# Kernel tuning notes

Measured on AMD Instinct MI355X. Metric: run time of the kernel, lower is better.

Reference implementation:

```python
import jax, jax.numpy as jnp
import numpy as np

B, C, H, W = 32, 1536, 24, 24
HID, D, K = 512, 128, 64  # hidden, cluster_dim, num_clusters


def setup_inputs() -> dict:
    key = jax.random.key(0)
    ks = jax.random.split(key, 6)
    def rn(k, shape, scale):
        return jax.random.normal(k, shape, dtype=jnp.float32) * scale
    return {
        "x": rn(ks[0], (B, C, H, W), 1.0),
        # cluster_features: Conv2d(C,512,1) -> ReLU -> Conv2d(512,D,1)
        "w1c": rn(ks[1], (HID, C), 0.02), "b1c": jnp.zeros((HID,), jnp.float32),
        "w2c": rn(ks[2], (D, HID), 0.02), "b2c": jnp.zeros((D,), jnp.float32),
        # score: Conv2d(C,512,1) -> ReLU -> Conv2d(512,K,1)
        "w1s": rn(ks[3], (HID, C), 0.02), "b1s": jnp.zeros((HID,), jnp.float32),
        "w2s": rn(ks[4], (K, HID), 0.02), "b2s": jnp.zeros((K,), jnp.float32),
        "temperature": jnp.array(1.0, jnp.float32),
    }


def _sinkhorn_log(S, num_iters=3):
    # log-domain OT solver with uniform marginals log(1/n), reg=1 (M/reg == M)
    b, m, n = S.shape
    norm = -jnp.log(jnp.asarray(n, S.dtype))
    log_a = jnp.full((b, m), norm, S.dtype)
    log_b = jnp.full((b, n), norm, S.dtype)
    u = jnp.zeros((b, m), S.dtype)
    v = jnp.zeros((b, n), S.dtype)
    for _ in range(num_iters):
        u = log_a - jax.nn.logsumexp(S + v[:, None, :], axis=2)
        v = log_b - jax.nn.logsumexp(S + u[:, :, None], axis=1)
    # get_matching_probs subtracts norm at the end
    return S + u[:, :, None] + v[:, None, :] - norm


def reference(x, w1c, b1c, w2c, b2c, w1s, b1s, w2s, b2s, temperature):
    b, c, h, w = x.shape
    xf = x.reshape(b, c, h * w)  # (B, C, N); 1x1 conv == channel GEMM
    # cluster features f: (B, D, N)
    hc = jax.nn.relu(jnp.einsum('oc,bcn->bon', w1c, xf) + b1c[None, :, None])
    f = jnp.einsum('oc,bcn->bon', w2c, hc) + b2c[None, :, None]
    # assignment scores p: (B, K, N)
    hs = jax.nn.relu(jnp.einsum('oc,bcn->bon', w1s, xf) + b1s[None, :, None])
    s = jnp.einsum('oc,bcn->bon', w2s, hs) + b2s[None, :, None]
    log_p = _sinkhorn_log(s, num_iters=3)
    p = jnp.exp(log_p / temperature) + jnp.exp(log_p)  # (B, K, N)
    # (f.unsqueeze(2) * p.unsqueeze(1)).sum(-1) == batched matmul
    agg = jnp.einsum('bcn,bkn->bck', f, p)  # (B, D, K)
    flat = agg.reshape(b, -1)
    nrm = jnp.maximum(jnp.linalg.norm(flat, axis=-1, keepdims=True), 1e-12)
    return flat / nrm
```

## Files before the change

kernel.cpp:

```cpp
#include <hip/hip_runtime.h>

typedef unsigned short ushort_t;
typedef float f32x4 __attribute__((ext_vector_type(4)));
typedef short short8 __attribute__((ext_vector_type(8)));

#define B_   32
#define C_   1536
#define N_   576
#define HID_ 512
#define D_   128
#define K_   64

__device__ __forceinline__ float bf2f(ushort_t u) {
    union { unsigned u; float f; } c; c.u = ((unsigned)u) << 16; return c.f;
}
__device__ __forceinline__ ushort_t f2bf(float x) {
    unsigned u = __float_as_uint(x);
    return (ushort_t)((u + 0x7FFFu + ((u >> 16) & 1u)) >> 16);
}

typedef const __attribute__((address_space(1))) char gas_char;
typedef __attribute__((address_space(3))) char las_char;
__device__ __forceinline__ void cp16(const void* g, void* l) {
    __builtin_amdgcn_global_load_lds((gas_char*)(size_t)g,
                                     (las_char*)(unsigned)(size_t)l, 16, 0, 0);
}
__device__ __forceinline__ void bar() {
    asm volatile("" ::: "memory");
    __builtin_amdgcn_s_barrier();
    asm volatile("" ::: "memory");
}

#define OB1_  1572864
#define OW2C_ 1573888
#define OB2C_ 1639424
#define OW2S_ 1639552
#define OB2S_ 1672320
#define WTOT_ 1672384
#define TRB2_ 3456
#define CVB4_ (((WTOT_ / 4) + 255) / 256)

__global__ __launch_bounds__(256) void prep_kernel(
    const void* __restrict__ x,
    const void* __restrict__ w1c, const void* __restrict__ b1c,
    const void* __restrict__ w2c, const void* __restrict__ b2c,
    const void* __restrict__ w1s, const void* __restrict__ b1s,
    const void* __restrict__ w2s, const void* __restrict__ b2s,
    const unsigned* __restrict__ temp,
    ushort_t* __restrict__ xt, ushort_t* __restrict__ o, float* __restrict__ Tp)
{
    __shared__ ushort_t t[128][65];
    unsigned d = temp[0];
    int flag = (d == 0x3F800000u) ? 1 : 0;
    int tid = threadIdx.x;
    int idx = blockIdx.x;
    if (idx == 0 && tid == 0)
        *Tp = flag ? __uint_as_float(d) : bf2f((ushort_t)(d & 0xFFFFu));

    if (idx < TRB2_) {
        int b = idx / 108, rem = idx % 108;
        int c0 = (rem % 12) * 128, n0 = (rem / 12) * 64;
        ushort_t* xtb = xt + (size_t)b * N_ * C_;
        int r = tid >> 4, n4 = (tid & 15) * 4;
        if (flag) {
            const float* xb = (const float*)x + (size_t)b * C_ * N_;
#pragma unroll
            for (int i = 0; i < 8; ++i) {
                int cc = r + i * 16;
                float4 v = *(const float4*)&xb[(size_t)(c0 + cc) * N_ + n0 + n4];
                t[cc][n4 + 0] = f2bf(v.x);
                t[cc][n4 + 1] = f2bf(v.y);
                t[cc][n4 + 2] = f2bf(v.z);
                t[cc][n4 + 3] = f2bf(v.w);
            }
        } else {
            const ushort_t* xb = (const ushort_t*)x + (size_t)b * C_ * N_;
#pragma unroll
            for (int i = 0; i < 8; ++i) {
                int cc = r + i * 16;
                *(uint2*)&t[cc][n4] =
                    *(const uint2*)&xb[(size_t)(c0 + cc) * N_ + n0 + n4];
            }
        }
        __syncthreads();
        int c8 = (tid & 15) * 8;
#pragma unroll
        for (int i = 0; i < 4; ++i) {
            int nn = r + i * 16;
            ushort_t vv[8];
#pragma unroll
            for (int j = 0; j < 8; ++j) vv[j] = t[c8 + j][nn];
            uint4 o4;
            o4.x = (unsigned)vv[0] | ((unsigned)vv[1] << 16);
            o4.y = (unsigned)vv[2] | ((unsigned)vv[3] << 16);
            o4.z = (unsigned)vv[4] | ((unsigned)vv[5] << 16);
            o4.w = (unsigned)vv[6] | ((unsigned)vv[7] << 16);
            *(uint4*)&xtb[(size_t)(n0 + nn) * C_ + c0 + c8] = o4;
        }
    } else {
        int i4 = ((idx - TRB2_) * 256 + tid) * 4;
        if (i4 >= WTOT_) return;
        const void* p; int off;
        if      (i4 < 786432)  { p = w1c; off = i4; }
        else if (i4 < OB1_)    { p = w1s; off = i4 - 786432; }
        else if (i4 < 1573376) { p = b1c; off = i4 - OB1_; }
        else if (i4 < OW2C_)   { p = b1s; off = i4 - 1573376; }
        else if (i4 < OB2C_)   { p = w2c; off = i4 - OW2C_; }
        else if (i4 < OW2S_)   { p = b2c; off = i4 - OB2C_; }
        else if (i4 < OB2S_)   { p = w2s; off = i4 - OW2S_; }
        else                   { p = b2s; off = i4 - OB2S_; }
        if (flag) {
            float4 v = *(const float4*)((const float*)p + off);
            uint2 r;
            r.x = (unsigned)f2bf(v.x) | ((unsigned)f2bf(v.y) << 16);
            r.y = (unsigned)f2bf(v.z) | ((unsigned)f2bf(v.w) << 16);
            *(uint2*)&o[i4] = r;
        } else {
            *(uint2*)&o[i4] = *(const uint2*)((const ushort_t*)p + off);
        }
    }
}

__global__ __launch_bounds__(256) void gemm1_kernel(
    const ushort_t* __restrict__ Xt, const ushort_t* __restrict__ W1,
    const ushort_t* __restrict__ bias, ushort_t* __restrict__ h)
{
    __shared__ ushort_t Atile[2][128 * 64];
    __shared__ ushort_t Btile[2][128 * 64];
    int idx = blockIdx.x;
    int l = (idx & 7) * 144 + (idx >> 3);
    int mt = l >> 3, t = l & 7;
    int row0 = mt * 128, col0 = t * 128;

    int tid = threadIdx.x, w = tid >> 6, lane = tid & 63;
    int wr = w >> 1, wc = w & 1;
    int r16 = lane & 15, q = lane >> 4, kh = q * 8;

    int srow = tid >> 3;
    int cx = ((tid & 7) ^ (srow & 7)) * 8;
    const ushort_t* ag[4];
    const ushort_t* bg[4];
#pragma unroll
    for (int s = 0; s < 4; ++s) {
        ag[s] = Xt + (size_t)(row0 + s * 32 + srow) * C_ + cx;
        bg[s] = W1 + (size_t)(col0 + s * 32 + srow) * C_ + cx;
    }

    f32x4 acc[4][4];
#pragma unroll
    for (int i = 0; i < 4; ++i)
#pragma unroll
        for (int j = 0; j < 4; ++j) acc[i][j] = f32x4{0.f, 0.f, 0.f, 0.f};

    int rowa = wr * 64 + r16;
    int rowb = wc * 64 + r16;
    int xr = (r16 & 7) * 8;

    auto stage = [&](int buf, int koff) {
#pragma unroll
        for (int s = 0; s < 4; ++s) {
            cp16(ag[s] + koff, &Atile[buf][tid * 8 + s * 2048]);
            cp16(bg[s] + koff, &Btile[buf][tid * 8 + s * 2048]);
        }
    };
    auto compute = [&](int cb) {
#pragma unroll
        for (int ks = 0; ks < 2; ++ks) {
            int ke = (ks * 32 + kh) ^ xr;
            short8 af[4], bf[4];
#pragma unroll
            for (int i = 0; i < 4; ++i)
                af[i] = *(const short8*)&Atile[cb][(rowa + i * 16) * 64 + ke];
#pragma unroll
            for (int j = 0; j < 4; ++j)
                bf[j] = *(const short8*)&Btile[cb][(rowb + j * 16) * 64 + ke];
#pragma unroll
            for (int i = 0; i < 4; ++i)
#pragma unroll
                for (int j = 0; j < 4; ++j)
                    acc[i][j] = __builtin_amdgcn_mfma_f32_16x16x32_bf16(
                        af[i], bf[j], acc[i][j], 0, 0, 0);
        }
    };

    stage(0, 0);
#pragma unroll
    for (int kt = 0; kt < 24; ++kt) {
        int buf = kt & 1;
        if (kt < 23) {
            stage(buf ^ 1, (kt + 1) * 64);
            asm volatile("s_waitcnt vmcnt(8)" ::: "memory");
        } else {
            asm volatile("s_waitcnt vmcnt(0)" ::: "memory");
        }
        bar();
        compute(buf);
        bar();
    }

#pragma unroll
    for (int j = 0; j < 4; ++j) {
        int col = col0 + wc * 64 + j * 16 + r16;
        float cb = bf2f(bias[col]);
#pragma unroll
        for (int i = 0; i < 4; ++i) {
            int rowo = row0 + wr * 64 + i * 16 + q * 4;
#pragma unroll
            for (int r = 0; r < 4; ++r) {
                float v = fmaxf(acc[i][j][r] + cb, 0.f);
                h[(size_t)(rowo + r) * 1024 + col] = f2bf(v);
            }
        }
    }
}

__global__ __launch_bounds__(256) void gemm2_kernel(
    const ushort_t* __restrict__ Wb, const ushort_t* __restrict__ h,
    ushort_t* __restrict__ fbuf, float* __restrict__ sbuf)
{
    __shared__ ushort_t Atile[2][128 * 32];
    __shared__ ushort_t Btile[2][128 * 32];
    int nt = blockIdx.x, b = blockIdx.y, z = blockIdx.z;
    int col0 = nt * 128;
    int Mclamp = z ? K_ : D_;
    const ushort_t* Aw   = Wb + (z ? OW2S_ : OW2C_);
    const ushort_t* bias = Wb + (z ? OB2S_ : OB2C_);
    const ushort_t* hb = h + (size_t)b * N_ * 1024 + (z ? 512 : 0);

    int tid = threadIdx.x, w = tid >> 6, lane = tid & 63;
    int wr = w >> 1, wc = w & 1;
    int r16 = lane & 15, q = lane >> 4, kh = q * 8;

    int srow = tid >> 2;
    int swz = ((tid & 3) ^ (srow & 3)) * 8;
    int ar0 = min(srow, Mclamp - 1);
    int ar1 = min(64 + srow, Mclamp - 1);
    const ushort_t* ag0 = Aw + (size_t)ar0 * HID_ + swz;
    const ushort_t* ag1 = Aw + (size_t)ar1 * HID_ + swz;
    int br0 = min(col0 + srow, N_ - 1);
    int br1 = min(col0 + 64 + srow, N_ - 1);
    const ushort_t* bg0 = hb + (size_t)br0 * 1024 + swz;
    const ushort_t* bg1 = hb + (size_t)br1 * 1024 + swz;

    f32x4 acc[4][4];
#pragma unroll
    for (int i = 0; i < 4; ++i)
#pragma unroll
        for (int j = 0; j < 4; ++j) acc[i][j] = f32x4{0.f, 0.f, 0.f, 0.f};

    int xr = (r16 & 3) * 8;

    auto stage = [&](int buf, int koff) {
        cp16(ag0 + koff, &Atile[buf][tid * 8]);
        cp16(ag1 + koff, &Atile[buf][2048 + tid * 8]);
        cp16(bg0 + koff, &Btile[buf][tid * 8]);
        cp16(bg1 + koff, &Btile[buf][2048 + tid * 8]);
    };
    auto compute = [&](int cb) {
        int ke = kh ^ xr;
        short8 af[4], bf[4];
#pragma unroll
        for (int i = 0; i < 4; ++i)
            af[i] = *(const short8*)&Atile[cb][(wr * 64 + i * 16 + r16) * 32 + ke];
#pragma unroll
        for (int j = 0; j < 4; ++j)
            bf[j] = *(const short8*)&Btile[cb][(wc * 64 + j * 16 + r16) * 32 + ke];
#pragma unroll
        for (int i = 0; i < 4; ++i)
#pragma unroll
            for (int j = 0; j < 4; ++j)
                acc[i][j] = __builtin_amdgcn_mfma_f32_16x16x32_bf16(
                    af[i], bf[j], acc[i][j], 0, 0, 0);
    };

    stage(0, 0);
#pragma unroll
    for (int kt = 0; kt < 16; ++kt) {
        int buf = kt & 1;
        if (kt < 15) {
            stage(buf ^ 1, (kt + 1) * 32);
            asm volatile("s_waitcnt vmcnt(4)" ::: "memory");
        } else {
            asm volatile("s_waitcnt vmcnt(0)" ::: "memory");
        }
        bar();
        compute(buf);
        bar();
    }

#pragma unroll
    for (int j = 0; j < 4; ++j) {
        int col = col0 + wc * 64 + j * 16 + r16;
#pragma unroll
        for (int i = 0; i < 4; ++i) {
            int rowb = wr * 64 + i * 16 + q * 4;
#pragma unroll
            for (int r = 0; r < 4; ++r) {
                int rr = rowb + r;
                if (rr < Mclamp && col < N_) {
                    float v = acc[i][j][r] + bf2f(bias[rr]);
                    if (z == 0)
                        fbuf[(size_t)b * D_ * N_ + (size_t)rr * N_ + col] = f2bf(v);
                    else
                        sbuf[(size_t)b * K_ * N_ + (size_t)rr * N_ + col] = v;
                }
            }
        }
    }
}

__global__ __launch_bounds__(512) void sinkhorn_kernel(
    const float* __restrict__ s_all, const float* __restrict__ Tp,
    ushort_t* __restrict__ P_all)
{
    int b = blockIdx.x;
    const float* S = s_all + (size_t)b * K_ * N_;
    __shared__ float Sl[K_ * 577];
    __shared__ float su[K_];
    __shared__ float sv[N_];
    int tid = threadIdx.x, w = tid >> 6, lane = tid & 63;
    const float norm = -logf((float)N_);

    const float4* S4 = (const float4*)S;
    for (int g = tid; g < (K_ * N_) / 4; g += 512) {
        float4 v = S4[g];
        int w0 = g * 4;
        int r = w0 / N_;
        int base = w0 + r;
        Sl[base + 0] = v.x; Sl[base + 1] = v.y;
        Sl[base + 2] = v.z; Sl[base + 3] = v.w;
    }
    for (int n = tid; n < N_; n += 512) sv[n] = 0.f;
    __syncthreads();

    for (int it = 0; it < 3; ++it) {
        for (int r = w; r < K_; r += 8) {
            const float* Sr = Sl + r * 577;
            float a0 = 0.f, a1 = 0.f, a2 = 0.f;
#pragma unroll
            for (int k = 0; k < 9; k += 3) {
                int n0 = lane + 64 * k;
                a0 += __expf(Sr[n0] + sv[n0]);
                a1 += __expf(Sr[n0 + 64] + sv[n0 + 64]);
                a2 += __expf(Sr[n0 + 128] + sv[n0 + 128]);
            }
            float t = a0 + a1 + a2;
#pragma unroll
            for (int off = 32; off; off >>= 1) t += __shfl_xor(t, off);
            if (lane == 0) su[r] = norm - __logf(t);
        }
        __syncthreads();
        for (int n = tid; n < N_; n += 512) {
            const float* Sc = Sl + n;
            float a0 = 0.f, a1 = 0.f, a2 = 0.f, a3 = 0.f;
#pragma unroll
            for (int m = 0; m < K_; m += 4) {
                a0 += __expf(Sc[(m + 0) * 577] + su[m + 0]);
                a1 += __expf(Sc[(m + 1) * 577] + su[m + 1]);
                a2 += __expf(Sc[(m + 2) * 577] + su[m + 2]);
                a3 += __expf(Sc[(m + 3) * 577] + su[m + 3]);
            }
            sv[n] = norm - __logf((a0 + a1) + (a2 + a3));
        }
        __syncthreads();
    }

    float invT = 1.f / (*Tp);
    ushort_t* Pb = P_all + (size_t)b * K_ * N_;
    for (int r = w; r < K_; r += 8) {
        float ur = su[r];
        const float* Sr = Sl + r * 577;
#pragma unroll
        for (int k = 0; k < 9; ++k) {
            int n0 = lane + 64 * k;
            float lp = Sr[n0] + ur + sv[n0] - norm;
            Pb[r * N_ + n0] = f2bf(__expf(lp * invT) + __expf(lp));
        }
    }
}

__global__ __launch_bounds__(256) void aggnorm_kernel(
    const ushort_t* __restrict__ f_all, const ushort_t* __restrict__ P_all,
    const unsigned* __restrict__ temp, void* __restrict__ out)
{
    __shared__ ushort_t Atile[2][128 * 64];
    __shared__ ushort_t Ptile[2][64 * 64];
    __shared__ float red[4];
    int b = blockIdx.x;
    const ushort_t* F = f_all + (size_t)b * D_ * N_;
    const ushort_t* P = P_all + (size_t)b * K_ * N_;
    int tid = threadIdx.x, w = tid >> 6, lane = tid & 63;
    int wr = w >> 1, wc = w & 1;
    int r16 = lane & 15, q = lane >> 4, kh = q * 8;

    int srow = tid >> 3;
    int cx = ((tid & 7) ^ (srow & 7)) * 8;
    const ushort_t* fg[4];
    const ushort_t* pg[2];
#pragma unroll
    for (int s = 0; s < 4; ++s)
        fg[s] = F + (size_t)(s * 32 + srow) * N_ + cx;
#pragma unroll
    for (int s = 0; s < 2; ++s)
        pg[s] = P + (size_t)(s * 32 + srow) * N_ + cx;

    f32x4 acc[4][2];
#pragma unroll
    for (int i = 0; i < 4; ++i)
#pragma unroll
        for (int j = 0; j < 2; ++j) acc[i][j] = f32x4{0.f, 0.f, 0.f, 0.f};

    int rowa = wr * 64 + r16;
    int rowp = wc * 32 + r16;
    int xr = (r16 & 7) * 8;

    auto stage = [&](int buf, int koff) {
#pragma unroll
        for (int s = 0; s < 4; ++s)
            cp16(fg[s] + koff, &Atile[buf][tid * 8 + s * 2048]);
#pragma unroll
        for (int s = 0; s < 2; ++s)
            cp16(pg[s] + koff, &Ptile[buf][tid * 8 + s * 2048]);
    };
    auto compute = [&](int cb) {
#pragma unroll
        for (int ks = 0; ks < 2; ++ks) {
            int ke = (ks * 32 + kh) ^ xr;
            short8 af[4], pf[2];
#pragma unroll
            for (int i = 0; i < 4; ++i)
                af[i] = *(const short8*)&Atile[cb][(rowa + i * 16) * 64 + ke];
#pragma unroll
            for (int j = 0; j < 2; ++j)
                pf[j] = *(const short8*)&Ptile[cb][(rowp + j * 16) * 64 + ke];
#pragma unroll
            for (int i = 0; i < 4; ++i)
#pragma unroll
                for (int j = 0; j < 2; ++j)
                    acc[i][j] = __builtin_amdgcn_mfma_f32_16x16x32_bf16(
                        af[i], pf[j], acc[i][j], 0, 0, 0);
        }
    };

    stage(0, 0);
#pragma unroll
    for (int kt = 0; kt < 9; ++kt) {
        int buf = kt & 1;
        if (kt < 8) {
            stage(buf ^ 1, (kt + 1) * 64);
            asm volatile("s_waitcnt vmcnt(6)" ::: "memory");
        } else {
            asm volatile("s_waitcnt vmcnt(0)" ::: "memory");
        }
        bar();
        compute(buf);
        bar();
    }

    float ssq = 0.f;
#pragma unroll
    for (int i = 0; i < 4; ++i)
#pragma unroll
        for (int j = 0; j < 2; ++j)
#pragma unroll
            for (int r = 0; r < 4; ++r) { float v = acc[i][j][r]; ssq += v * v; }
#pragma unroll
    for (int off = 32; off; off >>= 1) ssq += __shfl_xor(ssq, off);
    if (lane == 0) red[w] = ssq;
    __syncthreads();
    float tot = red[0] + red[1] + red[2] + red[3];
    float inv = 1.f / fmaxf(sqrtf(tot), 1e-12f);
    int flag = (temp[0] == 0x3F800000u) ? 1 : 0;
#pragma unroll
    for (int i = 0; i < 4; ++i) {
#pragma unroll
        for (int j = 0; j < 2; ++j) {
            int col = wc * 32 + j * 16 + r16;
#pragma unroll
            for (int r = 0; r < 4; ++r) {
                int row = wr * 64 + i * 16 + q * 4 + r;
                float v = acc[i][j][r] * inv;
                size_t idx = (size_t)b * D_ * K_ + (size_t)row * K_ + col;
                if (flag) ((float*)out)[idx] = v;
                else      ((ushort_t*)out)[idx] = f2bf(v);
            }
        }
    }
}

extern "C" void kernel_launch(void* const* d_in, const int* in_sizes, int n_in,
                              void* d_out, int out_size, void* d_ws, size_t ws_size,
                              hipStream_t stream) {
    const void* x    = d_in[0];
    const void* w1c  = d_in[1];
    const void* b1c  = d_in[2];
    const void* w2c  = d_in[3];
    const void* b2c  = d_in[4];
    const void* w1s  = d_in[5];
    const void* b1s  = d_in[6];
    const void* w2s  = d_in[7];
    const void* b2s  = d_in[8];
    const unsigned* temp = (const unsigned*)d_in[9];

    char* ws = (char*)d_ws;
    float* Tp = (float*)ws;
    ushort_t* Wb = (ushort_t*)(ws + 256);
    size_t offXt = 256 + (((size_t)WTOT_ * 2 + 255) & ~(size_t)255);
    ushort_t* Xt = (ushort_t*)(ws + offXt);
    size_t xtBytes = (size_t)B_ * N_ * C_ * 2;
    ushort_t* h  = (ushort_t*)(ws + offXt + xtBytes);
    size_t o0 = offXt;
    ushort_t* fbuf = (ushort_t*)(ws + o0);  o0 += (size_t)B_ * D_ * N_ * 2;
    float*    sbuf = (float*)(ws + o0);     o0 += (size_t)B_ * K_ * N_ * 4;
    ushort_t* Pws  = (ushort_t*)(ws + o0);  o0 += (size_t)B_ * K_ * N_ * 2;

    prep_kernel<<<dim3(TRB2_ + CVB4_), 256, 0, stream>>>(
        x, w1c, b1c, w2c, b2c, w1s, b1s, w2s, b2s, temp, Xt, Wb, Tp);
    gemm1_kernel<<<dim3(1152), 256, 0, stream>>>(Xt, Wb, Wb + OB1_, h);
    gemm2_kernel<<<dim3(5, B_, 2), 256, 0, stream>>>(Wb, h, fbuf, sbuf);
    sinkhorn_kernel<<<dim3(B_), 512, 0, stream>>>(sbuf, Tp, Pws);
    aggnorm_kernel<<<dim3(B_), 256, 0, stream>>>(fbuf, Pws, temp, (void*)d_out);
}
```

Before: 302.4 us.

## Fuse Sinkhorn and aggregation-normalize kernels into one tail kernel

Merges the Sinkhorn kernel and the aggregation/normalization GEMM into a single 512-thread kernel per batch. The P matrix is kept in registers, then written into LDS by reusing the S buffer, instead of going through global memory. Only F tiles are streamed with double-buffered async copies. This removes one launch and the global round trip for P, at the cost of a larger LDS footprint. The GEMM is still limited to one block per batch, 32 blocks in total.

After: 302.9 us. Within noise of the previous version (+0.2%).

```diff
diff --git a/kernel.cpp b/kernel.cpp
--- a/kernel.cpp
+++ b/kernel.cpp
@@ -309,19 +309,24 @@
     }
 }
 
-__global__ __launch_bounds__(512) void sinkhorn_kernel(
-    const float* __restrict__ s_all, const float* __restrict__ Tp,
-    ushort_t* __restrict__ P_all)
+__global__ __launch_bounds__(512) void tail_kernel(
+    const ushort_t* __restrict__ f_all, const float* __restrict__ s_all,
+    const float* __restrict__ Tp, const unsigned* __restrict__ temp,
+    void* __restrict__ out)
 {
-    int b = blockIdx.x;
-    const float* S = s_all + (size_t)b * K_ * N_;
     __shared__ float Sl[K_ * 577];
     __shared__ float su[K_];
     __shared__ float sv[N_];
+    __shared__ float red[8];
+    ushort_t* Plds = (ushort_t*)Sl;
+    ushort_t* At0  = (ushort_t*)((char*)Sl + 81920);
+    ushort_t* At1  = (ushort_t*)((char*)Sl + 81920 + 16384);
+
+    int b = blockIdx.x;
     int tid = threadIdx.x, w = tid >> 6, lane = tid & 63;
     const float norm = -logf((float)N_);
 
-    const float4* S4 = (const float4*)S;
+    const float4* S4 = (const float4*)(s_all + (size_t)b * K_ * N_);
     for (int g = tid; g < (K_ * N_) / 4; g += 512) {
         float4 v = S4[g];
         int w0 = g * 4;
@@ -366,94 +371,78 @@
     }
 
     float invT = 1.f / (*Tp);
-    ushort_t* Pb = P_all + (size_t)b * K_ * N_;
-    for (int r = w; r < K_; r += 8) {
+    ushort_t pv[8][9];
+#pragma unroll
+    for (int rr = 0; rr < 8; ++rr) {
+        int r = w * 8 + rr;
         float ur = su[r];
         const float* Sr = Sl + r * 577;
 #pragma unroll
         for (int k = 0; k < 9; ++k) {
             int n0 = lane + 64 * k;
             float lp = Sr[n0] + ur + sv[n0] - norm;
-            Pb[r * N_ + n0] = f2bf(__expf(lp * invT) + __expf(lp));
-        }
-    }
-}
-
-__global__ __launch_bounds__(256) void aggnorm_kernel(
-    const ushort_t* __restrict__ f_all, const ushort_t* __restrict__ P_all,
-    const unsigned* __restrict__ temp, void* __restrict__ out)
-{
-    __shared__ ushort_t Atile[2][128 * 64];
-    __shared__ ushort_t Ptile[2][64 * 64];
-    __shared__ float red[4];
-    int b = blockIdx.x;
+            pv[rr][k] = f2bf(__expf(lp * invT) + __expf(lp));
+        }
+    }
+    __syncthreads();
+#pragma unroll
+    for (int rr = 0; rr < 8; ++rr) {
+        int r = w * 8 + rr;
+#pragma unroll
+        for (int k = 0; k < 9; ++k)
+            Plds[r * 584 + lane + 64 * k] = pv[rr][k];
+    }
+    __syncthreads();
+
+    int wr = w >> 2, wc = w & 3;
+    int r16 = lane & 15, q = lane >> 4, kh = q * 8;
     const ushort_t* F = f_all + (size_t)b * D_ * N_;
-    const ushort_t* P = P_all + (size_t)b * K_ * N_;
-    int tid = threadIdx.x, w = tid >> 6, lane = tid & 63;
-    int wr = w >> 1, wc = w & 1;
-    int r16 = lane & 15, q = lane >> 4, kh = q * 8;
-
     int srow = tid >> 3;
     int cx = ((tid & 7) ^ (srow & 7)) * 8;
-    const ushort_t* fg[4];
-    const ushort_t* pg[2];
-#pragma unroll
-    for (int s = 0; s < 4; ++s)
-        fg[s] = F + (size_t)(s * 32 + srow) * N_ + cx;
-#pragma unroll
-    for (int s = 0; s < 2; ++s)
-        pg[s] = P + (size_t)(s * 32 + srow) * N_ + cx;
-
-    f32x4 acc[4][2];
-#pragma unroll
-    for (int i = 0; i < 4; ++i)
-#pragma unroll
-        for (int j = 0; j < 2; ++j) acc[i][j] = f32x4{0.f, 0.f, 0.f, 0.f};
+    const ushort_t* fg0 = F + (size_t)srow * N_ + cx;
+    const ushort_t* fg1 = F + (size_t)(64 + srow) * N_ + cx;
+
+    f32x4 acc[4];
+#pragma unroll
+    for (int i = 0; i < 4; ++i) acc[i] = f32x4{0.f, 0.f, 0.f, 0.f};
 
     int rowa = wr * 64 + r16;
-    int rowp = wc * 32 + r16;
+    int prow = wc * 16 + r16;
     int xr = (r16 & 7) * 8;
 
-    auto stage = [&](int buf, int koff) {
-#pragma unroll
-        for (int s = 0; s < 4; ++s)
-            cp16(fg[s] + koff, &Atile[buf][tid * 8 + s * 2048]);
-#pragma unroll
-        for (int s = 0; s < 2; ++s)
-            cp16(pg[s] + koff, &Ptile[buf][tid * 8 + s * 2048]);
+    auto stageF = [&](ushort_t* At, int koff) {
+        cp16(fg0 + koff, At + tid * 8);
+        cp16(fg1 + koff, At + 4096 + tid * 8);
     };
-    auto compute = [&](int cb) {
+    auto computeT = [&](const ushort_t* At, int s) {
 #pragma unroll
         for (int ks = 0; ks < 2; ++ks) {
             int ke = (ks * 32 + kh) ^ xr;
-            short8 af[4], pf[2];
+            short8 af[4];
 #pragma unroll
             for (int i = 0; i < 4; ++i)
-                af[i] = *(const short8*)&Atile[cb][(rowa + i * 16) * 64 + ke];
-#pragma unroll
-            for (int j = 0; j < 2; ++j)
-                pf[j] = *(const short8*)&Ptile[cb][(rowp + j * 16) * 64 + ke];
+                af[i] = *(const short8*)&At[(rowa + i * 16) * 64 + ke];
+            short8 pf = *(const short8*)&Plds[prow * 584 + s * 64 + ks * 32 + kh];
 #pragma unroll
             for (int i = 0; i < 4; ++i)
-#pragma unroll
-                for (int j = 0; j < 2; ++j)
-                    acc[i][j] = __builtin_amdgcn_mfma_f32_16x16x32_bf16(
-                        af[i], pf[j], acc[i][j], 0, 0, 0);
+                acc[i] = __builtin_amdgcn_mfma_f32_16x16x32_bf16(
+                    af[i], pf, acc[i], 0, 0, 0);
         }
     };
 
-    stage(0, 0);
+    stageF(At0, 0);
 #pragma unroll
     for (int kt = 0; kt < 9; ++kt) {
-        int buf = kt & 1;
+        ushort_t* cb = (kt & 1) ? At1 : At0;
+        ushort_t* nb = (kt & 1) ? At0 : At1;
         if (kt < 8) {
-            stage(buf ^ 1, (kt + 1) * 64);
-            asm volatile("s_waitcnt vmcnt(6)" ::: "memory");
+            stageF(nb, (kt + 1) * 64);
+            asm volatile("s_waitcnt vmcnt(2)" ::: "memory");
         } else {
             asm volatile("s_waitcnt vmcnt(0)" ::: "memory");
         }
         bar();
-        compute(buf);
+        computeT(cb, kt);
         bar();
     }
 
@@ -461,29 +450,25 @@
 #pragma unroll
     for (int i = 0; i < 4; ++i)
 #pragma unroll
-        for (int j = 0; j < 2; ++j)
-#pragma unroll
-            for (int r = 0; r < 4; ++r) { float v = acc[i][j][r]; ssq += v * v; }
+        for (int r = 0; r < 4; ++r) { float v = acc[i][r]; ssq += v * v; }
 #pragma unroll
     for (int off = 32; off; off >>= 1) ssq += __shfl_xor(ssq, off);
     if (lane == 0) red[w] = ssq;
     __syncthreads();
-    float tot = red[0] + red[1] + red[2] + red[3];
+    float tot = (red[0] + red[1] + red[2] + red[3])
+              + (red[4] + red[5] + red[6] + red[7]);
     float inv = 1.f / fmaxf(sqrtf(tot), 1e-12f);
     int flag = (temp[0] == 0x3F800000u) ? 1 : 0;
 #pragma unroll
     for (int i = 0; i < 4; ++i) {
-#pragma unroll
-        for (int j = 0; j < 2; ++j) {
-            int col = wc * 32 + j * 16 + r16;
-#pragma unroll
-            for (int r = 0; r < 4; ++r) {
-                int row = wr * 64 + i * 16 + q * 4 + r;
-                float v = acc[i][j][r] * inv;
-                size_t idx = (size_t)b * D_ * K_ + (size_t)row * K_ + col;
-                if (flag) ((float*)out)[idx] = v;
-                else      ((ushort_t*)out)[idx] = f2bf(v);
-            }
+        int col = wc * 16 + r16;
+#pragma unroll
+        for (int r = 0; r < 4; ++r) {
+            int row = wr * 64 + i * 16 + q * 4 + r;
+            float v = acc[i][r] * inv;
+            size_t idx = (size_t)b * D_ * K_ + (size_t)row * K_ + col;
+            if (flag) ((float*)out)[idx] = v;
+            else      ((ushort_t*)out)[idx] = f2bf(v);
         }
     }
 }
@@ -512,12 +497,10 @@
     size_t o0 = offXt;
     ushort_t* fbuf = (ushort_t*)(ws + o0);  o0 += (size_t)B_ * D_ * N_ * 2;
     float*    sbuf = (float*)(ws + o0);     o0 += (size_t)B_ * K_ * N_ * 4;
-    ushort_t* Pws  = (ushort_t*)(ws + o0);  o0 += (size_t)B_ * K_ * N_ * 2;
 
     prep_kernel<<<dim3(TRB2_ + CVB4_), 256, 0, stream>>>(
         x, w1c, b1c, w2c, b2c, w1s, b1s, w2s, b2s, temp, Xt, Wb, Tp);
     gemm1_kernel<<<dim3(1152), 256, 0, stream>>>(Xt, Wb, Wb + OB1_, h);
     gemm2_kernel<<<dim3(5, B_, 2), 256, 0, stream>>>(Wb, h, fbuf, sbuf);
-    sinkhorn_kernel<<<dim3(B_), 512, 0, stream>>>(sbuf, Tp, Pws);
-    aggnorm_kernel<<<dim3(B_), 256, 0, stream>>>(fbuf, Pws, temp, (void*)d_out);
-}
+    tail_kernel<<<dim3(B_), 512, 0, stream>>>(fbuf, sbuf, Tp, temp, (void*)d_out);
+}
```
